# Performance work log

Measured on AMD Instinct MI355X. Metric: run time of the kernel, lower is better.

The kernel has to match this reference:

```python
import jax, jax.numpy as jnp
import numpy as np


def setup_inputs() -> dict:
    key = jax.random.key(0)
    k1, k2, k3 = jax.random.split(key, 3)
    B, H, W = 4, 1024, 1024
    GD, GH, GW = 8, 16, 16
    NIN, NOUT = 3, 3
    grid = jax.random.normal(k1, (B, (NIN + 1) * NOUT, GD, GH, GW), dtype=jnp.float32)
    guide = jax.random.uniform(k2, (B, 1, H, W), dtype=jnp.float32)  # in [0,1)
    image = jax.random.uniform(k3, (B, NIN, H, W), dtype=jnp.float32)
    return {"grid": grid, "guide": guide, "image": image}


def _bilateral_slice_apply(grid, guide, image):
    """HDRNet bilateral slice + per-pixel affine apply.

    grid:  [B, (n_in+1)*n_out, gd, gh, gw]
    guide: [B, 1, H, W], values in [0, 1]
    image: [B, n_in, H, W]
    out:   [B, n_out, H, W]
    """
    B, C, GD, GH, GW = grid.shape
    _, NIN, H, W = image.shape
    NOUT = C // (NIN + 1)

    # Continuous grid coordinates (HDRNet convention: sample at pixel centers,
    # shifted by -0.5 so tent weights are centered on grid cells).
    gx = (jnp.arange(W, dtype=jnp.float32) + 0.5) * (GW / W) - 0.5  # [W]
    gy = (jnp.arange(H, dtype=jnp.float32) + 0.5) * (GH / H) - 0.5  # [H]
    gz = guide[:, 0] * GD - 0.5                                      # [B,H,W]

    fx, fy, fz = jnp.floor(gx), jnp.floor(gy), jnp.floor(gz)

    def gather_corner(g, zi, yi, xi):
        # g: [C,gd,gh,gw]; zi: [H,W]; yi: [H]; xi: [W] -> [C,H,W]
        return g[:, zi, yi[:, None], xi[None, :]]

    gather_b = jax.vmap(gather_corner, in_axes=(0, 0, None, None))

    acc = jnp.zeros((B, C, H, W), dtype=grid.dtype)
    for dz in (0.0, 1.0):
        zf = fz + dz
        wz = jnp.maximum(1.0 - jnp.abs(zf - gz), 0.0)               # [B,H,W]
        zi = jnp.clip(zf, 0, GD - 1).astype(jnp.int32)
        for dy in (0.0, 1.0):
            yf = fy + dy
            wy = jnp.maximum(1.0 - jnp.abs(yf - gy), 0.0)           # [H]
            yi = jnp.clip(yf, 0, GH - 1).astype(jnp.int32)
            for dx in (0.0, 1.0):
                xf = fx + dx
                wx = jnp.maximum(1.0 - jnp.abs(xf - gx), 0.0)       # [W]
                xi = jnp.clip(xf, 0, GW - 1).astype(jnp.int32)
                w = wz * (wy[:, None] * wx[None, :])                # [B,H,W]
                corner = gather_b(grid, zi, yi, xi)                 # [B,C,H,W]
                acc = acc + w[:, None] * corner

    # Per-pixel affine: out[o] = sum_j A[o,j] * in[j] + A[o,n_in]
    coeffs = acc.reshape(B, NOUT, NIN + 1, H, W)
    out = jnp.einsum('bojhw,bjhw->bohw', coeffs[:, :, :NIN], image) + coeffs[:, :, NIN]
    return out


def reference(grid, guide, image):
    return _bilateral_slice_apply(grid, guide, image)
```

## Files before the change

kernel.cpp:

```cpp
#include <hip/hip_runtime.h>
#include <hip/hip_fp16.h>

#define BATCH 4
#define HH 1024
#define WW 1024
#define GDp 8
#define NC 12
#define PAIR2 12
#define NPAIR 21
#define HROW2 268

typedef float f4 __attribute__((ext_vector_type(4)));
union V4 { int4 i4; __half2 h[4]; };

__global__ __launch_bounds__(256, 4) void bsa_kernel(
    const float* __restrict__ grid,
    const float* __restrict__ guide,
    const float* __restrict__ image,
    float* __restrict__ out)
{
    __shared__ float sg[GDp][3][3][NC];
    __shared__ __align__(16) __half2 Hs2[16][HROW2];

    const int bx = blockIdx.x;
    const int by = blockIdx.y;
    const int b  = blockIdx.z;
    const int tx = threadIdx.x;
    const int ty = threadIdx.y;
    const int tid = ty * 16 + tx;

    const int x0 = bx * 64;
    const int y0 = by * 16;
    const float inv64 = 1.0f / 64.0f;

    const float gy0 = (y0 + 0.5f) * inv64 - 0.5f;
    const int ylo = (int)floorf(gy0);

    const int y = y0 + ty;
    const int xloc = 4 * tx;
    const size_t plane = (size_t)HH * WW;
    const size_t gpix = ((size_t)(b * HH + y)) * WW + x0 + xloc;
    const size_t ib   = (size_t)b * 3 * plane + (size_t)y * WW + x0 + xloc;
    const float4 g4  = *(const float4*)&guide[gpix];
    const float4 im0 = *(const float4*)&image[ib];
    const float4 im1 = *(const float4*)&image[ib + plane];
    const float4 im2 = *(const float4*)&image[ib + 2 * plane];

    {
        const int z = tid >> 5;
        const int u = tid & 31;
        if (u < 27) {
            const int cell = (u * 11) >> 5;
            const int cq   = u - cell * 3;
            const int yy   = (cell * 11) >> 5;
            const int xx   = cell - yy * 3;
            const int gxi = min(max(bx - 1 + xx, 0), 15);
            const int gyi = min(max(ylo + yy, 0), 15);
            const float* gp = grid + (size_t)b * (NC * GDp * 256)
                                   + ((size_t)z * 16 + gyi) * 16 + gxi;
#pragma unroll
            for (int j = 0; j < 4; ++j) {
                const int c = cq * 4 + j;
                const int pos = (c < 8) ? ((c & 3) * 2 + (c >> 2)) : c;
                sg[z][yy][xx][pos] = gp[(size_t)c * (GDp * 256)];
            }
        }
    }
    __syncthreads();

    for (int e = tid; e < 384; e += 256) {
        const int r    = e & 15;
        const int cell = e >> 4;
        const int xs   = cell >> 3;
        const int z    = cell & 7;
        const float gy  = (y0 + r + 0.5f) * inv64 - 0.5f;
        const float fyf = floorf(gy);
        const float wy1 = gy - fyf;
        const float wy0 = 1.0f - wy1;
        const int ys0 = (int)fyf - ylo;
        const float* s0 = &sg[z][ys0][xs][0];
        const float* s1 = &sg[z][ys0 + 1][xs][0];
        __half2 h[6];
#pragma unroll
        for (int m = 0; m < 6; ++m) {
            h[m] = __floats2half2_rn(wy0 * s0[2*m]   + wy1 * s1[2*m],
                                     wy0 * s0[2*m+1] + wy1 * s1[2*m+1]);
        }
        __half2* rowp = &Hs2[r][0];
        if (z < 7) {
            __half2* hd = rowp + (xs * 7 + z) * PAIR2;
#pragma unroll
            for (int m = 0; m < 6; ++m) hd[m] = h[m];
        }
        if (z > 0) {
            __half2* hd = rowp + (xs * 7 + (z - 1)) * PAIR2 + 6;
#pragma unroll
            for (int m = 0; m < 6; ++m) hd[m] = h[m];
        }
    }
    __syncthreads();

    const int xs0 = tx >> 3;
    const float fxf = (float)(bx - 1 + xs0);
    const float gxb = (x0 + xloc + 0.5f) * inv64 - 0.5f;
    const __half2* Hrow = &Hs2[ty][0];

    const float gk[4]  = {g4.x, g4.y, g4.z, g4.w};
    const float ia[4]  = {im0.x, im0.y, im0.z, im0.w};
    const float ja[4]  = {im1.x, im1.y, im1.z, im1.w};
    const float ka[4]  = {im2.x, im2.y, im2.z, im2.w};
    float ok0[4], ok1[4], ok2[4];

    const __half oneh = __float2half_rn(1.0f);

#pragma unroll
    for (int k = 0; k < 4; ++k) {
        const float wx1 = (gxb - fxf) + (float)k * inv64;
        const float wx0 = 1.0f - wx1;

        const float gz  = fmaf(gk[k], 8.0f, -0.5f);
        const float fzf = floorf(gz);
        const float zpf = fminf(fmaxf(fzf, 0.0f), 6.0f);
        const float whi = fminf(fmaxf(gz - zpf, 0.0f), 1.0f);
        const float wlo = 1.0f - whi;
        const int zp = (int)zpf;

        const __half2 w00 = __float2half2_rn(wx0 * wlo);
        const __half2 w10 = __float2half2_rn(wx0 * whi);
        const __half2 w01 = __float2half2_rn(wx1 * wlo);
        const __half2 w11 = __float2half2_rn(wx1 * whi);

        const __half2* q = Hrow + (xs0 * 7 + zp) * PAIR2;
        V4 va, vb, vc, vd, ve, vf;
        va.i4 = *(const int4*)(q);
        vb.i4 = *(const int4*)(q + 4);
        vc.i4 = *(const int4*)(q + 8);
        vd.i4 = *(const int4*)(q + 7 * PAIR2);
        ve.i4 = *(const int4*)(q + 7 * PAIR2 + 4);
        vf.i4 = *(const int4*)(q + 7 * PAIR2 + 8);

        const __half2 A0 = va.h[0], A1 = va.h[1], A2 = va.h[2], A3 = va.h[3];
        const __half2 A4 = vb.h[0], A5 = vb.h[1];
        const __half2 B0 = vb.h[2], B1 = vb.h[3];
        const __half2 B2 = vc.h[0], B3 = vc.h[1], B4 = vc.h[2], B5 = vc.h[3];
        const __half2 C0 = vd.h[0], C1 = vd.h[1], C2 = vd.h[2], C3 = vd.h[3];
        const __half2 C4 = ve.h[0], C5 = ve.h[1];
        const __half2 D0 = ve.h[2], D1 = ve.h[3];
        const __half2 D2 = vf.h[0], D3 = vf.h[1], D4 = vf.h[2], D5 = vf.h[3];

        const __half2 r0 = __hfma2(w00, A0, __hfma2(w10, B0, __hfma2(w01, C0, __hmul2(w11, D0))));
        const __half2 r1 = __hfma2(w00, A1, __hfma2(w10, B1, __hfma2(w01, C1, __hmul2(w11, D1))));
        const __half2 r2 = __hfma2(w00, A2, __hfma2(w10, B2, __hfma2(w01, C2, __hmul2(w11, D2))));
        const __half2 r3 = __hfma2(w00, A3, __hfma2(w10, B3, __hfma2(w01, C3, __hmul2(w11, D3))));
        const __half2 r4 = __hfma2(w00, A4, __hfma2(w10, B4, __hfma2(w01, C4, __hmul2(w11, D4))));
        const __half2 r5 = __hfma2(w00, A5, __hfma2(w10, B5, __hfma2(w01, C5, __hmul2(w11, D5))));

        const __half i0h = __float2half_rn(ia[k]);
        const __half i1h = __float2half_rn(ja[k]);
        const __half i2h = __float2half_rn(ka[k]);
        const __half2 bi0 = __half2half2(i0h);
        const __half2 bi1 = __half2half2(i1h);
        const __half2 bi2 = __half2half2(i2h);

        const __half2 acc01 = __hfma2(bi0, r0, __hfma2(bi1, r1, __hfma2(bi2, r2, r3)));
        const __half2 d2 = __hfma2(__halves2half2(i0h, i1h), r4,
                                   __hmul2(__halves2half2(i2h, oneh), r5));

        ok0[k] = __low2float(acc01);
        ok1[k] = __high2float(acc01);
        ok2[k] = __half2float(__hadd(__low2half(d2), __high2half(d2)));
    }

    *(float4*)&out[ib]             = make_float4(ok0[0], ok0[1], ok0[2], ok0[3]);
    *(float4*)&out[ib + plane]     = make_float4(ok1[0], ok1[1], ok1[2], ok1[3]);
    *(float4*)&out[ib + 2 * plane] = make_float4(ok2[0], ok2[1], ok2[2], ok2[3]);
}

extern "C" void kernel_launch(void* const* d_in, const int* in_sizes, int n_in,
                              void* d_out, int out_size, void* d_ws, size_t ws_size,
                              hipStream_t stream) {
    const float* grid  = (const float*)d_in[0];
    const float* guide = (const float*)d_in[1];
    const float* image = (const float*)d_in[2];
    float* out = (float*)d_out;

    dim3 block(16, 16, 1);
    dim3 grid_dim(WW / 64, HH / 16, BATCH);
    bsa_kernel<<<grid_dim, block, 0, stream>>>(grid, guide, image, out);
}
```

Measured before the change: 25.06 us.

## Process four row tiles per block with double-buffered slice table and prefetch

Each block now covers 64 rows instead of 16, looping over four 16-row tiles. The grid-cell staging into shared memory happens once per block. The half-precision y-interpolated table is double-buffered, and the next tile's guide and image values are prefetched while the current tile computes. This amortises the per-block grid gather and launch overhead and tries to overlap global loads with compute, at the cost of four times fewer blocks and more shared memory per block.

```diff
diff --git a/kernel.cpp b/kernel.cpp
--- a/kernel.cpp
+++ b/kernel.cpp
@@ -7,10 +7,9 @@
 #define GDp 8
 #define NC 12
 #define PAIR2 12
-#define NPAIR 21
 #define HROW2 268
-
-typedef float f4 __attribute__((ext_vector_type(4)));
+#define NTILE 4
+
 union V4 { int4 i4; __half2 h[4]; };
 
 __global__ __launch_bounds__(256, 4) void bsa_kernel(
@@ -20,31 +19,31 @@
     float* __restrict__ out)
 {
     __shared__ float sg[GDp][3][3][NC];
-    __shared__ __align__(16) __half2 Hs2[16][HROW2];
-
-    const int bx = blockIdx.x;
-    const int by = blockIdx.y;
-    const int b  = blockIdx.z;
+    __shared__ __align__(16) __half2 Hs2[2][16][HROW2];
+
+    const int bx  = blockIdx.x;
+    const int byc = blockIdx.y;
+    const int b   = blockIdx.z;
     const int tx = threadIdx.x;
     const int ty = threadIdx.y;
     const int tid = ty * 16 + tx;
 
-    const int x0 = bx * 64;
-    const int y0 = by * 16;
+    const int x0  = bx * 64;
+    const int y0c = byc * 64;
     const float inv64 = 1.0f / 64.0f;
 
-    const float gy0 = (y0 + 0.5f) * inv64 - 0.5f;
-    const int ylo = (int)floorf(gy0);
-
-    const int y = y0 + ty;
+    const float gy0c = (y0c + 0.5f) * inv64 - 0.5f;
+    const int ylo = (int)floorf(gy0c);
+
     const int xloc = 4 * tx;
     const size_t plane = (size_t)HH * WW;
-    const size_t gpix = ((size_t)(b * HH + y)) * WW + x0 + xloc;
-    const size_t ib   = (size_t)b * 3 * plane + (size_t)y * WW + x0 + xloc;
-    const float4 g4  = *(const float4*)&guide[gpix];
-    const float4 im0 = *(const float4*)&image[ib];
-    const float4 im1 = *(const float4*)&image[ib + plane];
-    const float4 im2 = *(const float4*)&image[ib + 2 * plane];
+    const size_t gpix0 = ((size_t)(b * HH + y0c + ty)) * WW + x0 + xloc;
+    const size_t ib0   = (size_t)b * 3 * plane + (size_t)(y0c + ty) * WW + x0 + xloc;
+
+    float4 cg  = *(const float4*)&guide[gpix0];
+    float4 ci0 = *(const float4*)&image[ib0];
+    float4 ci1 = *(const float4*)&image[ib0 + plane];
+    float4 ci2 = *(const float4*)&image[ib0 + 2 * plane];
 
     {
         const int z = tid >> 5;
@@ -68,112 +67,136 @@
     }
     __syncthreads();
 
-    for (int e = tid; e < 384; e += 256) {
-        const int r    = e & 15;
-        const int cell = e >> 4;
-        const int xs   = cell >> 3;
-        const int z    = cell & 7;
-        const float gy  = (y0 + r + 0.5f) * inv64 - 0.5f;
-        const float fyf = floorf(gy);
-        const float wy1 = gy - fyf;
-        const float wy0 = 1.0f - wy1;
-        const int ys0 = (int)fyf - ylo;
-        const float* s0 = &sg[z][ys0][xs][0];
-        const float* s1 = &sg[z][ys0 + 1][xs][0];
-        __half2 h[6];
-#pragma unroll
-        for (int m = 0; m < 6; ++m) {
-            h[m] = __floats2half2_rn(wy0 * s0[2*m]   + wy1 * s1[2*m],
-                                     wy0 * s0[2*m+1] + wy1 * s1[2*m+1]);
-        }
-        __half2* rowp = &Hs2[r][0];
-        if (z < 7) {
-            __half2* hd = rowp + (xs * 7 + z) * PAIR2;
-#pragma unroll
-            for (int m = 0; m < 6; ++m) hd[m] = h[m];
-        }
-        if (z > 0) {
-            __half2* hd = rowp + (xs * 7 + (z - 1)) * PAIR2 + 6;
-#pragma unroll
-            for (int m = 0; m < 6; ++m) hd[m] = h[m];
-        }
-    }
+    auto build_hs = [&](int buf, int t) {
+        for (int e = tid; e < 384; e += 256) {
+            const int r    = e & 15;
+            const int cell = e >> 4;
+            const int xs   = cell >> 3;
+            const int z    = cell & 7;
+            const float gy  = (y0c + t * 16 + r + 0.5f) * inv64 - 0.5f;
+            const float fyf = floorf(gy);
+            const float wy1 = gy - fyf;
+            const float wy0 = 1.0f - wy1;
+            const int ys0 = (int)fyf - ylo;
+            const float* s0 = &sg[z][ys0][xs][0];
+            const float* s1 = &sg[z][ys0 + 1][xs][0];
+            __half2 h[6];
+#pragma unroll
+            for (int m = 0; m < 6; ++m) {
+                h[m] = __floats2half2_rn(wy0 * s0[2*m]   + wy1 * s1[2*m],
+                                         wy0 * s0[2*m+1] + wy1 * s1[2*m+1]);
+            }
+            __half2* rowp = &Hs2[buf][r][0];
+            if (z < 7) {
+                __half2* hd = rowp + (xs * 7 + z) * PAIR2;
+#pragma unroll
+                for (int m = 0; m < 6; ++m) hd[m] = h[m];
+            }
+            if (z > 0) {
+                __half2* hd = rowp + (xs * 7 + (z - 1)) * PAIR2 + 6;
+#pragma unroll
+                for (int m = 0; m < 6; ++m) hd[m] = h[m];
+            }
+        }
+    };
+
+    build_hs(0, 0);
     __syncthreads();
 
     const int xs0 = tx >> 3;
     const float fxf = (float)(bx - 1 + xs0);
     const float gxb = (x0 + xloc + 0.5f) * inv64 - 0.5f;
-    const __half2* Hrow = &Hs2[ty][0];
-
-    const float gk[4]  = {g4.x, g4.y, g4.z, g4.w};
-    const float ia[4]  = {im0.x, im0.y, im0.z, im0.w};
-    const float ja[4]  = {im1.x, im1.y, im1.z, im1.w};
-    const float ka[4]  = {im2.x, im2.y, im2.z, im2.w};
-    float ok0[4], ok1[4], ok2[4];
-
     const __half oneh = __float2half_rn(1.0f);
 
 #pragma unroll
-    for (int k = 0; k < 4; ++k) {
-        const float wx1 = (gxb - fxf) + (float)k * inv64;
-        const float wx0 = 1.0f - wx1;
-
-        const float gz  = fmaf(gk[k], 8.0f, -0.5f);
-        const float fzf = floorf(gz);
-        const float zpf = fminf(fmaxf(fzf, 0.0f), 6.0f);
-        const float whi = fminf(fmaxf(gz - zpf, 0.0f), 1.0f);
-        const float wlo = 1.0f - whi;
-        const int zp = (int)zpf;
-
-        const __half2 w00 = __float2half2_rn(wx0 * wlo);
-        const __half2 w10 = __float2half2_rn(wx0 * whi);
-        const __half2 w01 = __float2half2_rn(wx1 * wlo);
-        const __half2 w11 = __float2half2_rn(wx1 * whi);
-
-        const __half2* q = Hrow + (xs0 * 7 + zp) * PAIR2;
-        V4 va, vb, vc, vd, ve, vf;
-        va.i4 = *(const int4*)(q);
-        vb.i4 = *(const int4*)(q + 4);
-        vc.i4 = *(const int4*)(q + 8);
-        vd.i4 = *(const int4*)(q + 7 * PAIR2);
-        ve.i4 = *(const int4*)(q + 7 * PAIR2 + 4);
-        vf.i4 = *(const int4*)(q + 7 * PAIR2 + 8);
-
-        const __half2 A0 = va.h[0], A1 = va.h[1], A2 = va.h[2], A3 = va.h[3];
-        const __half2 A4 = vb.h[0], A5 = vb.h[1];
-        const __half2 B0 = vb.h[2], B1 = vb.h[3];
-        const __half2 B2 = vc.h[0], B3 = vc.h[1], B4 = vc.h[2], B5 = vc.h[3];
-        const __half2 C0 = vd.h[0], C1 = vd.h[1], C2 = vd.h[2], C3 = vd.h[3];
-        const __half2 C4 = ve.h[0], C5 = ve.h[1];
-        const __half2 D0 = ve.h[2], D1 = ve.h[3];
-        const __half2 D2 = vf.h[0], D3 = vf.h[1], D4 = vf.h[2], D5 = vf.h[3];
-
-        const __half2 r0 = __hfma2(w00, A0, __hfma2(w10, B0, __hfma2(w01, C0, __hmul2(w11, D0))));
-        const __half2 r1 = __hfma2(w00, A1, __hfma2(w10, B1, __hfma2(w01, C1, __hmul2(w11, D1))));
-        const __half2 r2 = __hfma2(w00, A2, __hfma2(w10, B2, __hfma2(w01, C2, __hmul2(w11, D2))));
-        const __half2 r3 = __hfma2(w00, A3, __hfma2(w10, B3, __hfma2(w01, C3, __hmul2(w11, D3))));
-        const __half2 r4 = __hfma2(w00, A4, __hfma2(w10, B4, __hfma2(w01, C4, __hmul2(w11, D4))));
-        const __half2 r5 = __hfma2(w00, A5, __hfma2(w10, B5, __hfma2(w01, C5, __hmul2(w11, D5))));
-
-        const __half i0h = __float2half_rn(ia[k]);
-        const __half i1h = __float2half_rn(ja[k]);
-        const __half i2h = __float2half_rn(ka[k]);
-        const __half2 bi0 = __half2half2(i0h);
-        const __half2 bi1 = __half2half2(i1h);
-        const __half2 bi2 = __half2half2(i2h);
-
-        const __half2 acc01 = __hfma2(bi0, r0, __hfma2(bi1, r1, __hfma2(bi2, r2, r3)));
-        const __half2 d2 = __hfma2(__halves2half2(i0h, i1h), r4,
-                                   __hmul2(__halves2half2(i2h, oneh), r5));
-
-        ok0[k] = __low2float(acc01);
-        ok1[k] = __high2float(acc01);
-        ok2[k] = __half2float(__hadd(__low2half(d2), __high2half(d2)));
+    for (int t = 0; t < NTILE; ++t) {
+        float4 ng, ni0, ni1, ni2;
+        if (t < NTILE - 1) {
+            const size_t gp  = gpix0 + (size_t)(t + 1) * 16 * WW;
+            const size_t ibn = ib0   + (size_t)(t + 1) * 16 * WW;
+            ng  = *(const float4*)&guide[gp];
+            ni0 = *(const float4*)&image[ibn];
+            ni1 = *(const float4*)&image[ibn + plane];
+            ni2 = *(const float4*)&image[ibn + 2 * plane];
+        }
+
+        const __half2* Hrow = &Hs2[t & 1][ty][0];
+        const size_t ib = ib0 + (size_t)t * 16 * WW;
+
+        const float gk[4]  = {cg.x, cg.y, cg.z, cg.w};
+        const float ia[4]  = {ci0.x, ci0.y, ci0.z, ci0.w};
+        const float ja[4]  = {ci1.x, ci1.y, ci1.z, ci1.w};
+        const float ka[4]  = {ci2.x, ci2.y, ci2.z, ci2.w};
+        float ok0[4], ok1[4], ok2[4];
+
+#pragma unroll
+        for (int k = 0; k < 4; ++k) {
+            const float wx1 = (gxb - fxf) + (float)k * inv64;
+            const float wx0 = 1.0f - wx1;
+
+            const float gz  = fmaf(gk[k], 8.0f, -0.5f);
+            const float fzf = floorf(gz);
+            const float zpf = fminf(fmaxf(fzf, 0.0f), 6.0f);
+            const float whi = fminf(fmaxf(gz - zpf, 0.0f), 1.0f);
+            const float wlo = 1.0f - whi;
+            const int zp = (int)zpf;
+
+            const __half2 w00 = __float2half2_rn(wx0 * wlo);
+            const __half2 w10 = __float2half2_rn(wx0 * whi);
+            const __half2 w01 = __float2half2_rn(wx1 * wlo);
+            const __half2 w11 = __float2half2_rn(wx1 * whi);
+
+            const __half2* q = Hrow + (xs0 * 7 + zp) * PAIR2;
+            V4 va, vb, vc, vd, ve, vf;
+            va.i4 = *(const int4*)(q);
+            vb.i4 = *(const int4*)(q + 4);
+            vc.i4 = *(const int4*)(q + 8);
+            vd.i4 = *(const int4*)(q + 7 * PAIR2);
+            ve.i4 = *(const int4*)(q + 7 * PAIR2 + 4);
+            vf.i4 = *(const int4*)(q + 7 * PAIR2 + 8);
+
+            const __half2 A0 = va.h[0], A1 = va.h[1], A2 = va.h[2], A3 = va.h[3];
+            const __half2 A4 = vb.h[0], A5 = vb.h[1];
+            const __half2 B0 = vb.h[2], B1 = vb.h[3];
+            const __half2 B2 = vc.h[0], B3 = vc.h[1], B4 = vc.h[2], B5 = vc.h[3];
+            const __half2 C0 = vd.h[0], C1 = vd.h[1], C2 = vd.h[2], C3 = vd.h[3];
+            const __half2 C4 = ve.h[0], C5 = ve.h[1];
+            const __half2 D0 = ve.h[2], D1 = ve.h[3];
+            const __half2 D2 = vf.h[0], D3 = vf.h[1], D4 = vf.h[2], D5 = vf.h[3];
+
+            const __half2 r0 = __hfma2(w00, A0, __hfma2(w10, B0, __hfma2(w01, C0, __hmul2(w11, D0))));
+            const __half2 r1 = __hfma2(w00, A1, __hfma2(w10, B1, __hfma2(w01, C1, __hmul2(w11, D1))));
+            const __half2 r2 = __hfma2(w00, A2, __hfma2(w10, B2, __hfma2(w01, C2, __hmul2(w11, D2))));
+            const __half2 r3 = __hfma2(w00, A3, __hfma2(w10, B3, __hfma2(w01, C3, __hmul2(w11, D3))));
+            const __half2 r4 = __hfma2(w00, A4, __hfma2(w10, B4, __hfma2(w01, C4, __hmul2(w11, D4))));
+            const __half2 r5 = __hfma2(w00, A5, __hfma2(w10, B5, __hfma2(w01, C5, __hmul2(w11, D5))));
+
+            const __half i0h = __float2half_rn(ia[k]);
+            const __half i1h = __float2half_rn(ja[k]);
+            const __half i2h = __float2half_rn(ka[k]);
+            const __half2 bi0 = __half2half2(i0h);
+            const __half2 bi1 = __half2half2(i1h);
+            const __half2 bi2 = __half2half2(i2h);
+
+            const __half2 acc01 = __hfma2(bi0, r0, __hfma2(bi1, r1, __hfma2(bi2, r2, r3)));
+            const __half2 d2 = __hfma2(__halves2half2(i0h, i1h), r4,
+                                       __hmul2(__halves2half2(i2h, oneh), r5));
+
+            ok0[k] = __low2float(acc01);
+            ok1[k] = __high2float(acc01);
+            ok2[k] = __half2float(__hadd(__low2half(d2), __high2half(d2)));
+        }
+
+        *(float4*)&out[ib]             = make_float4(ok0[0], ok0[1], ok0[2], ok0[3]);
+        *(float4*)&out[ib + plane]     = make_float4(ok1[0], ok1[1], ok1[2], ok1[3]);
+        *(float4*)&out[ib + 2 * plane] = make_float4(ok2[0], ok2[1], ok2[2], ok2[3]);
+
+        if (t < NTILE - 1) {
+            build_hs((t + 1) & 1, t + 1);
+            __syncthreads();
+            cg = ng; ci0 = ni0; ci1 = ni1; ci2 = ni2;
+        }
     }
-
-    *(float4*)&out[ib]             = make_float4(ok0[0], ok0[1], ok0[2], ok0[3]);
-    *(float4*)&out[ib + plane]     = make_float4(ok1[0], ok1[1], ok1[2], ok1[3]);
-    *(float4*)&out[ib + 2 * plane] = make_float4(ok2[0], ok2[1], ok2[2], ok2[3]);
 }
 
 extern "C" void kernel_launch(void* const* d_in, const int* in_sizes, int n_in,
@@ -185,6 +208,6 @@
     float* out = (float*)d_out;
 
     dim3 block(16, 16, 1);
-    dim3 grid_dim(WW / 64, HH / 16, BATCH);
+    dim3 grid_dim(WW / 64, HH / 64, BATCH);
     bsa_kernel<<<grid_dim, block, 0, stream>>>(grid, guide, image, out);
 }
```

After: 24.89 us. Within noise of the previous version (-0.7%).
